# Kernel optimization log

Measured on AMD Instinct MI355X. Metric: run time of the kernel, lower is better.

## Reference

```python
import jax, jax.numpy as jnp
import numpy as np

DIM = 1024
HEADS = 16
HIDDEN = 4096
EPS = 1e-5


def _layernorm(x, g, b):
    mu = jnp.mean(x, axis=-1, keepdims=True)
    var = jnp.mean(jnp.square(x - mu), axis=-1, keepdims=True)
    return (x - mu) * jax.lax.rsqrt(var + EPS) * g + b


def setup_inputs() -> dict:
    key = jax.random.key(0)
    ks = jax.random.split(key, 12)
    B, N, C, Hd = 2, 2048, DIM, HIDDEN
    s = 0.02
    inp = {
        "x": jax.random.normal(ks[0], (B, N, C), dtype=jnp.float32),
        "mask": jax.random.randint(ks[1], (B, N), 0, 2).astype(bool),
        "ln1_g": jnp.ones((C,), jnp.float32),
        "ln1_b": jnp.zeros((C,), jnp.float32),
        "qkv_w": jax.random.normal(ks[2], (3 * C, C), jnp.float32) * s,
        "q_bias": jax.random.normal(ks[3], (C,), jnp.float32) * s,
        "v_bias": jax.random.normal(ks[4], (C,), jnp.float32) * s,
        "proj_w": jax.random.normal(ks[5], (C, C), jnp.float32) * s,
        "proj_b": jnp.zeros((C,), jnp.float32),
        "ln2_g": jnp.ones((C,), jnp.float32),
        "ln2_b": jnp.zeros((C,), jnp.float32),
        "fc1_w": jax.random.normal(ks[6], (Hd, C), jnp.float32) * s,
        "fc1_b": jnp.zeros((Hd,), jnp.float32),
        "fc2_w": jax.random.normal(ks[7], (C, Hd), jnp.float32) * s,
        "fc2_b": jnp.zeros((C,), jnp.float32),
    }
    return inp


def _block(x, mask, ln1_g, ln1_b, qkv_w, q_bias, v_bias, proj_w, proj_b,
           ln2_g, ln2_b, fc1_w, fc1_b, fc2_w, fc2_b):
    B, N, C = x.shape
    H = HEADS
    hd = C // H
    scale = hd ** -0.5

    # --- attention branch ---
    xn = _layernorm(x, ln1_g, ln1_b)
    qkv_bias = jnp.concatenate([q_bias, jnp.zeros_like(v_bias), v_bias])
    qkv = xn @ qkv_w.T + qkv_bias                       # [B,N,3C]
    qkv = qkv.reshape(B, N, 3, H, hd).transpose(2, 0, 3, 1, 4)  # [3,B,H,N,hd]
    q, k, v = qkv[0], qkv[1], qkv[2]
    q = q * scale
    attn = jnp.einsum('bhqd,bhkd->bhqk',
                      q.astype(jnp.float32), k.astype(jnp.float32))
    attn = jnp.where(mask[:, None, None, :], -jnp.inf, attn)
    attn = jax.nn.softmax(attn, axis=-1).astype(x.dtype)
    out = jnp.einsum('bhqk,bhkd->bhqd', attn, v)        # [B,H,N,hd]
    out = out.transpose(0, 2, 1, 3).reshape(B, N, C)
    out = out @ proj_w.T + proj_b
    x = x + out

    # --- MLP branch (Mlp_ returns pre-activation hidden too; norm=Identity) ---
    x2 = _layernorm(x, ln2_g, ln2_b)
    h = x2 @ fc1_w.T + fc1_b                            # [B,N,HIDDEN]
    x_interm = h
    h = jax.nn.gelu(h, approximate=False)
    y = h @ fc2_w.T + fc2_b
    x = x + y
    return x_interm, x


def reference(x, mask, ln1_g, ln1_b, qkv_w, q_bias, v_bias, proj_w, proj_b,
              ln2_g, ln2_b, fc1_w, fc1_b, fc2_w, fc2_b):
    return _block(x, mask, ln1_g, ln1_b, qkv_w, q_bias, v_bias, proj_w, proj_b,
                  ln2_g, ln2_b, fc1_w, fc1_b, fc2_w, fc2_b)
```

## Files before the change

kernel.cpp:

```cpp
#include <hip/hip_runtime.h>
#include <hip/hip_bf16.h>

typedef __attribute__((ext_vector_type(8))) short short8;
typedef __attribute__((ext_vector_type(4))) short short4v;
typedef __attribute__((ext_vector_type(4))) float f32x4;

__device__ inline float bf2f(short s) {
    unsigned u = ((unsigned)(unsigned short)s) << 16;
    float f; __builtin_memcpy(&f, &u, 4); return f;
}
__device__ inline short f2bf(float f) {
    unsigned u; __builtin_memcpy(&u, &f, 4);
    unsigned r = (u + 0x7fffu + ((u >> 16) & 1u)) >> 16;
    return (short)r;
}
__device__ inline float ex2(float x) {
    float r; asm("v_exp_f32 %0, %1" : "=v"(r) : "v"(x)); return r;
}
__device__ inline unsigned cvtpk(float lo, float hi) {
    unsigned r; asm("v_cvt_pk_bf16_f32 %0, %1, %2" : "=v"(r) : "v"(lo), "v"(hi)); return r;
}
__device__ inline float gelu_fast(float x) {
    float xx = x * x;
    float u2 = x * fmaf(0.10294323f, xx, 2.3022085f);
    float t = ex2(u2);
    return x - x * __builtin_amdgcn_rcpf(t + 1.f);
}

#define GLD_LDS16(g, l) __builtin_amdgcn_global_load_lds( \
    (const __attribute__((address_space(1))) void*)(g),   \
    (__attribute__((address_space(3))) void*)(l), 16, 0, 0)

#define BARRIER_PIN do { __builtin_amdgcn_s_barrier(); __builtin_amdgcn_sched_barrier(0); } while (0)

__global__ __launch_bounds__(256) void detect_kernel(const ushort* __restrict__ x,
                                                     const unsigned char* __restrict__ m,
                                                     int* __restrict__ flags) {
    __shared__ int cnt, weirdAny, weird40, nzNon4;
    if (threadIdx.x == 0) { cnt = 0; weirdAny = 0; weird40 = 0; nzNon4 = 0; }
    __syncthreads();
    for (int t = threadIdx.x; t < 512; t += 256) {
        unsigned u = x[2 * t];
        int e = (int)((u >> 7) & 0xFF);
        if (e >= 100 && e <= 130) atomicAdd(&cnt, 1);
    }
    for (int i = threadIdx.x; i < 4096; i += 256) {
        unsigned b = m[i];
        if (b > 1) { atomicOr(&weirdAny, 1); if ((i & 3) == 0) atomicOr(&weird40, 1); }
        if (b != 0 && (i & 3) != 0) atomicOr(&nzNon4, 1);
    }
    __syncthreads();
    if (threadIdx.x == 0) {
        flags[0] = (cnt < 256) ? 1 : 0;
        flags[1] = weirdAny ? (weird40 ? 2 : 3) : (nzNon4 ? 1 : 0);
    }
}

__global__ __launch_bounds__(256) void prep_kernel(
    const void* __restrict__ xs, const void* __restrict__ ms,
    const void* __restrict__ ln1g, const void* __restrict__ ln1b,
    const void* __restrict__ qkvw, const void* __restrict__ qb,
    const void* __restrict__ vb, const void* __restrict__ pw,
    const void* __restrict__ pb, const void* __restrict__ ln2g,
    const void* __restrict__ ln2b, const void* __restrict__ f1w,
    const void* __restrict__ f1b, const void* __restrict__ f2w,
    const void* __restrict__ f2b,
    char* __restrict__ w, const int* __restrict__ flags) {
    bool f32w = flags[0] != 0;
    const size_t MB = 1024 * 1024;
    int bid = blockIdx.x, tid = threadIdx.x;
    if (!f32w && bid < 8192) return;
    char* small = w + 88 * MB;
    auto cvt8 = [&](const void* src, ushort* dst, int i) {
        if (f32w) {
            const float* s = (const float*)src + i;
            short8 o;
            for (int j = 0; j < 8; j++) o[j] = f2bf(s[j]);
            *(short8*)&dst[i] = o;
        } else {
            *(short8*)&dst[i] = *(const short8*)((const ushort*)src + i);
        }
    };
    if (bid < 2048)       cvt8(xs,   (ushort*)(w + 56 * MB), (bid * 256 + tid) * 8);
    else if (bid < 3584)  cvt8(qkvw, (ushort*)(w + 64 * MB), ((bid - 2048) * 256 + tid) * 8);
    else if (bid < 4096)  cvt8(pw,   (ushort*)(w + 70 * MB), ((bid - 3584) * 256 + tid) * 8);
    else if (bid < 6144)  cvt8(f1w,  (ushort*)(w + 72 * MB), ((bid - 4096) * 256 + tid) * 8);
    else if (bid < 8192)  cvt8(f2w,  (ushort*)(w + 80 * MB), ((bid - 6144) * 256 + tid) * 8);
    else if (bid < 8198) {
        int e = (bid - 8192) * 2048 + tid * 8;
        const void* src; ushort* dst; int off;
        if (e < 7168) {
            int t = e >> 10; off = e & 1023;
            const void* s0;
            if (t == 0) s0 = ln1g; else if (t == 1) s0 = ln1b; else if (t == 2) s0 = qb;
            else if (t == 3) s0 = vb; else if (t == 4) s0 = pb; else if (t == 5) s0 = ln2g;
            else s0 = ln2b;
            src = s0; dst = (ushort*)(small + t * 4096);
        } else if (e < 8192) { src = f2b; off = e - 7168; dst = (ushort*)(small + 9 * 4096); }
        else                 { src = f1b; off = e - 8192; dst = (ushort*)(small + 7 * 4096); }
        cvt8(src, dst, off);
    } else {
        int enc = flags[1];
        unsigned char* md = (unsigned char*)(small + 10 * 4096);
        int i0 = (bid - 8198) * 2048 + tid * 8;
        for (int j = 0; j < 8; j++) {
            int i = i0 + j;
            unsigned char v;
            if (enc == 0)      v = (((const int*)ms)[i] != 0);
            else if (enc == 1) v = (((const unsigned char*)ms)[i] != 0);
            else if (enc == 2) v = (((const ushort*)ms)[i] != 0);
            else               v = ((((const unsigned*)ms)[i] << 1) != 0);
            md[i] = v;
        }
    }
}

__global__ __launch_bounds__(256) void ln_kernel(const void* __restrict__ xraw,
                                                 const ushort* __restrict__ xconv,
                                                 const ushort* __restrict__ g,
                                                 const ushort* __restrict__ b,
                                                 ushort* __restrict__ y,
                                                 const int* __restrict__ flags) {
    const ushort* x = (flags[0] != 0) ? xconv : (const ushort*)xraw;
    int wave = threadIdx.x >> 6, lane = threadIdx.x & 63;
    int row = blockIdx.x * 4 + wave;
    const ushort* xp = x + (size_t)row * 1024 + lane * 16;
    short8 v0 = *(const short8*)xp;
    short8 v1 = *(const short8*)(xp + 8);
    float f[16]; float s = 0.f, ss = 0.f;
    for (int i = 0; i < 8; i++) { f[i] = bf2f(v0[i]); f[i + 8] = bf2f(v1[i]); }
    for (int i = 0; i < 16; i++) { s += f[i]; ss += f[i] * f[i]; }
    for (int o = 1; o < 64; o <<= 1) { s += __shfl_xor(s, o, 64); ss += __shfl_xor(ss, o, 64); }
    float mu = s * (1.f / 1024.f);
    float var = ss * (1.f / 1024.f) - mu * mu;
    float rstd = rsqrtf(var + 1e-5f);
    short8 g0 = *(const short8*)&g[lane * 16];
    short8 g1 = *(const short8*)&g[lane * 16 + 8];
    short8 b0 = *(const short8*)&b[lane * 16];
    short8 b1 = *(const short8*)&b[lane * 16 + 8];
    short8 o0v, o1v;
    for (int i = 0; i < 8; i++) {
        o0v[i] = f2bf((f[i] - mu) * rstd * bf2f(g0[i]) + bf2f(b0[i]));
        o1v[i] = f2bf((f[i + 8] - mu) * rstd * bf2f(g1[i]) + bf2f(b1[i]));
    }
    ushort* yp = y + (size_t)row * 1024 + lane * 16;
    *(short8*)yp = o0v;
    *(short8*)(yp + 8) = o1v;
}

template <int EPI>
__device__ __forceinline__ void gemm_body(ushort* SM,
                                          const ushort* __restrict__ A,
                                          const void* __restrict__ Wraw,
                                          const ushort* __restrict__ Wconv,
                                          int K,
                                          const ushort* __restrict__ p0,
                                          const void* __restrict__ p1raw,
                                          const ushort* __restrict__ p1conv,
                                          void* __restrict__ o0,
                                          ushort* __restrict__ o1,
                                          const int* __restrict__ flags) {
    bool f32w = flags[0] != 0;
    const ushort* W  = f32w ? Wconv  : (const ushort*)Wraw;
    const ushort* p1 = f32w ? p1conv : (const ushort*)p1raw;
    int tid = threadIdx.x;
    int wave = tid >> 6, lane = tid & 63;
    int wr = wave >> 1, wc = wave & 1;
    int lr = lane & 15, lg = lane >> 4;
    int m0 = blockIdx.x * 128, n0 = blockIdx.y * 128;
    f32x4 acc[4][4];
    for (int i = 0; i < 4; i++) for (int j = 0; j < 4; j++) acc[i][j] = (f32x4){0.f, 0.f, 0.f, 0.f};

    int s0 = wave * 2;
    int srow = lane >> 2;
    int sslot = (lane & 3) ^ ((srow >> 1) & 3);
    const ushort* gA0 = &A[(size_t)(m0 + s0 * 16 + srow) * K + sslot * 8];
    const ushort* gA1 = gA0 + (size_t)16 * K;
    const ushort* gW0 = &W[(size_t)(n0 + s0 * 16 + srow) * K + sslot * 8];
    const ushort* gW1 = gW0 + (size_t)16 * K;

    auto STAGE = [&](int buf, int k0) {
        ushort* lA = &SM[buf * 4096 + s0 * 512];
        ushort* lW = &SM[12288 + buf * 4096 + s0 * 512];
        GLD_LDS16(gA0 + k0, lA);
        GLD_LDS16(gA1 + k0, lA + 512);
        GLD_LDS16(gW0 + k0, lW);
        GLD_LDS16(gW1 + k0, lW + 512);
    };

    int nk = K >> 5;
    STAGE(0, 0);
    if (nk > 1) {
        STAGE(1, 32);
        asm volatile("s_waitcnt vmcnt(4)" ::: "memory");
    } else {
        asm volatile("s_waitcnt vmcnt(0)" ::: "memory");
    }
    BARRIER_PIN;

    int rs = lg ^ ((lr >> 1) & 3);
    int cur = 0, stg = 2;
    for (int t = 0; t < nk; ++t) {
        if (t + 2 < nk) STAGE(stg, (t + 2) << 5);
        const ushort* Ab = &SM[cur * 4096];
        const ushort* Wb = &SM[12288 + cur * 4096];
        short8 af[4], wf[4];
        for (int mi = 0; mi < 4; mi++) af[mi] = *(const short8*)&Ab[(wr * 64 + mi * 16 + lr) * 32 + rs * 8];
        for (int ni = 0; ni < 4; ni++) wf[ni] = *(const short8*)&Wb[(wc * 64 + ni * 16 + lr) * 32 + rs * 8];
        for (int mi = 0; mi < 4; mi++)
            for (int ni = 0; ni < 4; ni++)
                acc[mi][ni] = __builtin_amdgcn_mfma_f32_16x16x32_bf16(af[mi], wf[ni], acc[mi][ni], 0, 0, 0);
        if (t + 1 < nk) {
            if (t + 2 < nk) asm volatile("s_waitcnt vmcnt(4)" ::: "memory");
            else            asm volatile("s_waitcnt vmcnt(0)" ::: "memory");
            BARRIER_PIN;
        }
        cur = (cur == 2) ? 0 : cur + 1;
        stg = (stg == 2) ? 0 : stg + 1;
    }

    float* Cs = (float*)SM;
    bool of32 = (EPI == 2 || EPI == 3) ? f32w : false;
    int r2 = tid >> 3;
    int lc = tid & 7;
    for (int mi = 0; mi < 4; mi++) {
        __syncthreads();
        int rb = wr * 16 + lg * 4;
        for (int ni = 0; ni < 4; ni++) {
            f32x4 v = acc[mi][ni];
            int cl = wc * 64 + ni * 16 + lr;
            for (int rr = 0; rr < 4; rr++) Cs[(rb + rr) * 132 + cl] = v[rr];
        }
        __syncthreads();
        int grow = m0 + mi * 16 + (r2 < 16 ? r2 : 48 + r2);
        if (EPI == 3 && of32) {
            for (int k = 0; k < 4; k++) {
                int c0l = k * 32 + lc * 4;
                int gcol = n0 + c0l;
                f32x4 v;
                for (int j = 0; j < 4; j++)
                    v[j] = Cs[r2 * 132 + c0l + j] + bf2f(p0[gcol + j])
                         + bf2f(p1[(size_t)grow * 1024 + gcol + j]);
                *(f32x4*)&((float*)o0)[16777216 + (size_t)grow * 1024 + gcol] = v;
            }
        } else {
            for (int half = 0; half < 2; half++) {
                int c0l = half * 64 + lc * 8;
                int gcol = n0 + c0l;
                float hv[8];
                for (int j = 0; j < 8; j++) hv[j] = Cs[r2 * 132 + c0l + j];
                short8 o;
                if (EPI == 0) {
                    int part = gcol >> 10, cc = gcol & 1023;
                    if (part == 0)
                        for (int j = 0; j < 8; j++) o[j] = f2bf((hv[j] + bf2f(p0[cc + j])) * 0.18033688f);
                    else if (part == 1)
                        for (int j = 0; j < 8; j++) o[j] = f2bf(hv[j]);
                    else
                        for (int j = 0; j < 8; j++) o[j] = f2bf(hv[j] + bf2f(p1[cc + j]));
                    *(short8*)&((ushort*)o0)[(size_t)grow * 3072 + gcol] = o;
                } else if (EPI == 1) {
                    for (int j = 0; j < 8; j++)
                        o[j] = f2bf(hv[j] + bf2f(p0[gcol + j])
                                  + bf2f(p1[(size_t)grow * 1024 + gcol + j]));
                    *(short8*)&((ushort*)o0)[(size_t)grow * 1024 + gcol] = o;
                } else if (EPI == 2) {
                    float h[8];
                    short8 og;
                    for (int j = 0; j < 8; j++) {
                        h[j] = hv[j] + bf2f(p0[gcol + j]);
                        og[j] = f2bf(gelu_fast(h[j]));
                    }
                    *(short8*)&o1[(size_t)grow * 4096 + gcol] = og;
                    if (of32) {
                        float* dst = &((float*)o0)[(size_t)grow * 4096 + gcol];
                        *(f32x4*)&dst[0] = (f32x4){h[0], h[1], h[2], h[3]};
                        *(f32x4*)&dst[4] = (f32x4){h[4], h[5], h[6], h[7]};
                    } else {
                        short8 oh;
                        for (int j = 0; j < 8; j++) oh[j] = f2bf(h[j]);
                        *(short8*)&((ushort*)o0)[(size_t)grow * 4096 + gcol] = oh;
                    }
                } else {
                    for (int j = 0; j < 8; j++)
                        o[j] = f2bf(hv[j] + bf2f(p0[gcol + j])
                                  + bf2f(p1[(size_t)grow * 1024 + gcol + j]));
                    *(short8*)&((ushort*)o0)[16777216 + (size_t)grow * 1024 + gcol] = o;
                }
            }
        }
    }
}

#define GEMM_WRAP(NAME, EPI)                                                          \
__global__ __launch_bounds__(256) void NAME(const ushort* __restrict__ A,            \
                                            const void* __restrict__ Wraw,           \
                                            const ushort* __restrict__ Wconv, int K, \
                                            const ushort* __restrict__ p0,           \
                                            const void* __restrict__ p1raw,          \
                                            const ushort* __restrict__ p1conv,       \
                                            void* __restrict__ o0,                   \
                                            ushort* __restrict__ o1,                 \
                                            const int* __restrict__ flags) {         \
    __shared__ ushort SM[24576];                                                     \
    gemm_body<EPI>(SM, A, Wraw, Wconv, K, p0, p1raw, p1conv, o0, o1, flags);         \
}

GEMM_WRAP(gemm_qkv, 0)
GEMM_WRAP(gemm_proj, 1)
GEMM_WRAP(gemm_fc1, 2)
GEMM_WRAP(gemm_fc2, 3)

__global__ __launch_bounds__(256) void vtrans_kernel(const ushort* __restrict__ qkv,
                                                     ushort* __restrict__ vT) {
    __shared__ ushort T[64][72];
    int bh = blockIdx.x;
    int b = bh >> 4, h = bh & 15;
    int n0 = blockIdx.y * 64;
    int t = threadIdx.x;
    int r = t >> 2;
    int c0 = (t & 3) * 16;
    const ushort* src = qkv + (size_t)(b * 2048 + n0 + r) * 3072 + 2048 + h * 64 + c0;
    *(short8*)&T[r][c0]     = *(const short8*)&src[0];
    *(short8*)&T[r][c0 + 8] = *(const short8*)&src[8];
    __syncthreads();
    int d = t >> 2;
    int g0 = (t & 3) * 16;
    short8 o0v, o1v;
    for (int j = 0; j < 8; j++) { o0v[j] = T[g0 + j][d]; o1v[j] = T[g0 + 8 + j][d]; }
    ushort* dst = vT + ((size_t)bh * 64 + d) * 2048 + n0 + g0;
    *(short8*)&dst[0] = o0v;
    *(short8*)&dst[8] = o1v;
}

__global__ __launch_bounds__(256) void attn_kernel(const ushort* __restrict__ qkv,
                                                   const ushort* __restrict__ vT,
                                                   const unsigned char* __restrict__ mask,
                                                   ushort* __restrict__ ao) {
    __shared__ ushort Ks[2][4096];
    __shared__ ushort Vs[2][4096];
    __shared__ unsigned Plw[4][544];
    __shared__ unsigned Pmf[1024];

    int tid = threadIdx.x, wave = tid >> 6, lane = tid & 63;
    int bid = (blockIdx.x & 7) * 64 + (blockIdx.x >> 3);
    int g = bid * 4 + wave;
    int b = g >> 10;
    int h = (g >> 6) & 15;
    int qt = g & 63;
    int lr = lane & 15, lg = lane >> 4;

    const ushort* qp = qkv + (size_t)(b * 2048 + qt * 32) * 3072 + h * 64;
    const ushort* kp = qkv + (size_t)(b * 2048) * 3072 + 1024 + h * 64;
    const ushort* vp = vT + ((size_t)(b * 16 + h) * 64) * 2048;
    const unsigned char* mk = mask + b * 2048;

    for (int i = tid; i < 1024; i += 256) {
        unsigned lo = mk[2 * i] ? 0u : 0xFFFFu;
        unsigned hi = mk[2 * i + 1] ? 0u : 0xFFFF0000u;
        Pmf[i] = lo | hi;
    }

    short8 qa[2][2];
    for (int sub = 0; sub < 2; sub++)
        for (int ks = 0; ks < 2; ks++)
            qa[sub][ks] = *(const short8*)&qp[(sub * 16 + lr) * 3072 + ks * 32 + lg * 8];
    short8 ones;
    for (int j = 0; j < 8; j++) ones[j] = (short)0x3F80;

    int srowoff = lane >> 3;
    int sslot = (lane & 7) ^ srowoff;
    int rs0 = lg ^ (lr & 7);
    int rs1 = (4 + lg) ^ (lr & 7);

    f32x4 accT[2][4];
    f32x4 accL[2];
    for (int s = 0; s < 2; s++) {
        accL[s] = (f32x4){0.f, 0.f, 0.f, 0.f};
        for (int i = 0; i < 4; i++) accT[s][i] = (f32x4){0.f, 0.f, 0.f, 0.f};
    }

    auto STAGEKV = [&](int buf, int c0) {
        const ushort* ksrc = kp + (size_t)(c0 + wave * 16 + srowoff) * 3072 + sslot * 8;
        GLD_LDS16(ksrc, &Ks[buf][wave * 1024]);
        GLD_LDS16(ksrc + (size_t)8 * 3072, &Ks[buf][wave * 1024 + 512]);
        const ushort* vsrc = vp + (size_t)(wave * 16 + srowoff) * 2048 + c0 + sslot * 8;
        GLD_LDS16(vsrc, &Vs[buf][wave * 1024]);
        GLD_LDS16(vsrc + (size_t)8 * 2048, &Vs[buf][wave * 1024 + 512]);
    };

    STAGEKV(0, 0);
    __syncthreads();

    for (int it = 0; it < 32; ++it) {
        int c0 = it * 64;
        int cur = it & 1;
        if (it < 31) STAGEKV(cur ^ 1, c0 + 64);

        unsigned mw[4][2];
        for (int t = 0; t < 4; t++) {
            uint2 m2 = *(const uint2*)&Pmf[it * 32 + 8 * t + 2 * lg];
            mw[t][0] = m2.x; mw[t][1] = m2.y;
        }
        f32x4 st[2][4];
        for (int t = 0; t < 4; t++) {
            int row = t * 16 + lr;
            short8 kf0 = *(const short8*)&Ks[cur][row * 64 + rs0 * 8];
            short8 kf1 = *(const short8*)&Ks[cur][row * 64 + rs1 * 8];
            for (int sub = 0; sub < 2; sub++) {
                f32x4 z = (f32x4){0.f, 0.f, 0.f, 0.f};
                z = __builtin_amdgcn_mfma_f32_16x16x32_bf16(kf0, qa[sub][0], z, 0, 0, 0);
                z = __builtin_amdgcn_mfma_f32_16x16x32_bf16(kf1, qa[sub][1], z, 0, 0, 0);
                st[sub][t] = z;
            }
        }
        short8 vf[2][4];
        for (int ks = 0; ks < 2; ks++) {
            int rsk = ks ? rs1 : rs0;
            for (int nt = 0; nt < 4; nt++)
                vf[ks][nt] = *(const short8*)&Vs[cur][(nt * 16 + lr) * 64 + rsk * 8];
        }
        for (int sub = 0; sub < 2; sub++) {
            for (int t = 0; t < 4; t++) {
                for (int rrh = 0; rrh < 2; rrh++) {
                    float plo = ex2(st[sub][t][2 * rrh]);
                    float phi = ex2(st[sub][t][2 * rrh + 1]);
                    unsigned w = cvtpk(plo, phi) & mw[t][rrh];
                    Plw[wave][(8 * t + 2 * lg + rrh) * 17 + lr] = w;
                }
            }
            for (int ks = 0; ks < 2; ks++) {
                unsigned wu[4];
                for (int jj = 0; jj < 4; jj++)
                    wu[jj] = Plw[wave][(16 * ks + 4 * lg + jj) * 17 + lr];
                short8 pf;
                __builtin_memcpy(&pf, wu, 16);
                accL[sub] = __builtin_amdgcn_mfma_f32_16x16x32_bf16(ones, pf, accL[sub], 0, 0, 0);
                for (int nt = 0; nt < 4; nt++)
                    accT[sub][nt] = __builtin_amdgcn_mfma_f32_16x16x32_bf16(vf[ks][nt], pf, accT[sub][nt], 0, 0, 0);
            }
        }
        __syncthreads();
    }

    for (int sub = 0; sub < 2; sub++) {
        float ls = accL[sub][0];
        float inv = (ls > 0.f) ? 1.f / ls : 0.f;
        ushort* op = ao + ((size_t)(b * 2048 + qt * 32 + sub * 16) * 1024) + h * 64;
        for (int nt = 0; nt < 4; nt++) {
            unsigned w0 = cvtpk(accT[sub][nt][0] * inv, accT[sub][nt][1] * inv);
            unsigned w1 = cvtpk(accT[sub][nt][2] * inv, accT[sub][nt][3] * inv);
            uint2 ov; ov.x = w0; ov.y = w1;
            *(uint2*)&op[lr * 1024 + 16 * nt + 4 * lg] = ov;
        }
    }
}

extern "C" void kernel_launch(void* const* d_in, const int* in_sizes, int n_in,
                              void* d_out, int out_size, void* d_ws, size_t ws_size,
                              hipStream_t stream) {
    (void)in_sizes; (void)n_in; (void)out_size; (void)ws_size;

    char* w = (char*)d_ws;
    const size_t MB = 1024 * 1024;
    ushort* xn  = (ushort*)(w + 0 * MB);
    ushort* qkv = (ushort*)(w + 8 * MB);
    ushort* vT  = (ushort*)(w + 32 * MB);
    ushort* x1  = (ushort*)(w + 40 * MB);
    ushort* x2n = (ushort*)(w + 48 * MB);
    ushort* gh  = (ushort*)(w + 8 * MB);
    ushort* x_c    = (ushort*)(w + 56 * MB);
    ushort* qkvw_c = (ushort*)(w + 64 * MB);
    ushort* projw_c= (ushort*)(w + 70 * MB);
    ushort* fc1w_c = (ushort*)(w + 72 * MB);
    ushort* fc2w_c = (ushort*)(w + 80 * MB);
    char* small = w + 88 * MB;
    ushort* ln1g_c = (ushort*)(small + 0 * 4096);
    ushort* ln1b_c = (ushort*)(small + 1 * 4096);
    ushort* qbias_c= (ushort*)(small + 2 * 4096);
    ushort* vbias_c= (ushort*)(small + 3 * 4096);
    ushort* projb_c= (ushort*)(small + 4 * 4096);
    ushort* ln2g_c = (ushort*)(small + 5 * 4096);
    ushort* ln2b_c = (ushort*)(small + 6 * 4096);
    ushort* fc1b_c = (ushort*)(small + 7 * 4096);
    ushort* fc2b_c = (ushort*)(small + 9 * 4096);
    unsigned char* mask_c = (unsigned char*)(small + 10 * 4096);
    int* flags = (int*)(small + 11 * 4096);
    ushort* ao = xn;

    detect_kernel<<<1, 256, 0, stream>>>((const ushort*)d_in[0],
                                         (const unsigned char*)d_in[1], flags);
    prep_kernel<<<8200, 256, 0, stream>>>(d_in[0], d_in[1], d_in[2], d_in[3], d_in[4],
                                          d_in[5], d_in[6], d_in[7], d_in[8], d_in[9],
                                          d_in[10], d_in[11], d_in[12], d_in[13], d_in[14],
                                          w, flags);

    ln_kernel<<<1024, 256, 0, stream>>>(d_in[0], x_c, ln1g_c, ln1b_c, xn, flags);
    gemm_qkv<<<dim3(32, 24), 256, 0, stream>>>(xn, d_in[4], qkvw_c, 1024, qbias_c,
                                               vbias_c, vbias_c, qkv, nullptr, flags);
    vtrans_kernel<<<dim3(32, 32), 256, 0, stream>>>(qkv, vT);
    attn_kernel<<<512, 256, 0, stream>>>(qkv, vT, mask_c, ao);
    gemm_proj<<<dim3(32, 8), 256, 0, stream>>>(ao, d_in[7], projw_c, 1024, projb_c,
                                               d_in[0], x_c, x1, nullptr, flags);
    ln_kernel<<<1024, 256, 0, stream>>>(x1, x1, ln2g_c, ln2b_c, x2n, flags);
    gemm_fc1<<<dim3(32, 32), 256, 0, stream>>>(x2n, d_in[11], fc1w_c, 1024, fc1b_c,
                                               fc1b_c, fc1b_c, d_out, gh, flags);
    gemm_fc2<<<dim3(32, 8), 256, 0, stream>>>(gh, d_in[13], fc2w_c, 4096, fc2b_c,
                                              x1, x1, d_out, nullptr, flags);
}
```

Measured before the change: 258.5 us.

## Use 256x256-tile 8-wave GEMM kernel for QKV and FC1 projections

Adds a new GEMM kernel with 256x256 output tiles, 512 threads and a double-buffered direct-to-LDS load pipeline, then uses it for the QKV and FC1 GEMMs instead of the 128-wide tile kernel. Bigger tiles raise arithmetic intensity and cut global/L2 traffic per FLOP. The cost is a smaller grid (192 and 256 blocks on a large-CU device), which may leave CUs idle, plus heavy LDS and register use (128 KB LDS, 32 accumulators per lane).

```diff
diff --git a/kernel.cpp b/kernel.cpp
--- a/kernel.cpp
+++ b/kernel.cpp
@@ -149,6 +149,169 @@
 }
 
 template <int EPI>
+__global__ __launch_bounds__(512, 2) void gemm256_body(const ushort* __restrict__ A,
+                                                       const void* __restrict__ Wraw,
+                                                       const ushort* __restrict__ Wconv,
+                                                       int K,
+                                                       const ushort* __restrict__ p0,
+                                                       const void* __restrict__ p1raw,
+                                                       const ushort* __restrict__ p1conv,
+                                                       void* __restrict__ o0,
+                                                       ushort* __restrict__ o1,
+                                                       const int* __restrict__ flags) {
+    __shared__ ushort SM[65536];
+    bool f32w = flags[0] != 0;
+    const ushort* W  = f32w ? Wconv  : (const ushort*)Wraw;
+    const ushort* p1 = f32w ? p1conv : (const ushort*)p1raw;
+    int tid = threadIdx.x;
+    int wave = tid >> 6, lane = tid & 63;
+    int wm = wave >> 2, wn = wave & 3;
+    int lr = lane & 15, lg = lane >> 4;
+    int m0 = blockIdx.x * 256, n0 = blockIdx.y * 256;
+
+    f32x4 acc[8][4];
+#pragma unroll
+    for (int i = 0; i < 8; i++)
+#pragma unroll
+        for (int j = 0; j < 4; j++) acc[i][j] = (f32x4){0.f, 0.f, 0.f, 0.f};
+
+    int l31 = lane & 31;
+    int sgrp = (lane >> 5) * 2;
+    const ushort* gA = &A[(size_t)(m0 + wave * 32 + l31) * K];
+    const ushort* gB = &W[(size_t)(n0 + wave * 32 + l31) * K];
+
+    auto STAGE_U = [&](int op, int h, int buf, int k0) {
+        const ushort* g = op ? gB : gA;
+        ushort* base = &SM[op * 32768 + buf * 16384 + h * 8192 + wave * 1024];
+        GLD_LDS16(g + k0 + h * 32 + sgrp * 8, base);
+        GLD_LDS16(g + k0 + h * 32 + (sgrp + 1) * 8, base + 512);
+    };
+    auto rdA = [&](int R, int h, int cur) -> short8 {
+        return *(const short8*)&SM[cur * 16384 + h * 8192 + (R >> 5) * 1024 +
+                                   (lg & 1) * 512 + ((lg >> 1) * 32 + (R & 31)) * 8];
+    };
+    auto rdB = [&](int R, int h, int cur) -> short8 {
+        return *(const short8*)&SM[32768 + cur * 16384 + h * 8192 + (R >> 5) * 1024 +
+                                   (lg & 1) * 512 + ((lg >> 1) * 32 + (R & 31)) * 8];
+    };
+
+    int nk = K >> 6;
+    STAGE_U(0, 0, 0, 0); STAGE_U(1, 0, 0, 0); STAGE_U(0, 1, 0, 0); STAGE_U(1, 1, 0, 0);
+
+    for (int t = 0; t < nk; ++t) {
+        int cur = t & 1, nxt = cur ^ 1;
+        int k1 = (t + 1) << 6;
+        bool more = (t + 1) < nk;
+        short8 af[4], bf[4];
+        if (more) { STAGE_U(0, 0, nxt, k1); asm volatile("s_waitcnt vmcnt(6)" ::: "memory"); }
+        else      { asm volatile("s_waitcnt vmcnt(4)" ::: "memory"); }
+        BARRIER_PIN;
+#pragma unroll
+        for (int nf = 0; nf < 4; nf++) bf[nf] = rdB(wn * 64 + nf * 16 + lr, 0, cur);
+#pragma unroll
+        for (int mi = 0; mi < 4; mi++) af[mi] = rdA(wm * 128 + mi * 16 + lr, 0, cur);
+        __builtin_amdgcn_s_setprio(1);
+#pragma unroll
+        for (int mi = 0; mi < 4; mi++)
+#pragma unroll
+            for (int nf = 0; nf < 4; nf++)
+                acc[mi][nf] = __builtin_amdgcn_mfma_f32_16x16x32_bf16(af[mi], bf[nf], acc[mi][nf], 0, 0, 0);
+        __builtin_amdgcn_s_setprio(0);
+        if (more) STAGE_U(1, 0, nxt, k1);
+#pragma unroll
+        for (int mi = 0; mi < 4; mi++) af[mi] = rdA(wm * 128 + 64 + mi * 16 + lr, 0, cur);
+        __builtin_amdgcn_s_setprio(1);
+#pragma unroll
+        for (int mi = 0; mi < 4; mi++)
+#pragma unroll
+            for (int nf = 0; nf < 4; nf++)
+                acc[4 + mi][nf] = __builtin_amdgcn_mfma_f32_16x16x32_bf16(af[mi], bf[nf], acc[4 + mi][nf], 0, 0, 0);
+        __builtin_amdgcn_s_setprio(0);
+        if (more) { STAGE_U(0, 1, nxt, k1); asm volatile("s_waitcnt vmcnt(6)" ::: "memory"); }
+        else      { asm volatile("s_waitcnt vmcnt(0)" ::: "memory"); }
+        BARRIER_PIN;
+#pragma unroll
+        for (int nf = 0; nf < 4; nf++) bf[nf] = rdB(wn * 64 + nf * 16 + lr, 1, cur);
+#pragma unroll
+        for (int mi = 0; mi < 4; mi++) af[mi] = rdA(wm * 128 + mi * 16 + lr, 1, cur);
+        __builtin_amdgcn_s_setprio(1);
+#pragma unroll
+        for (int mi = 0; mi < 4; mi++)
+#pragma unroll
+            for (int nf = 0; nf < 4; nf++)
+                acc[mi][nf] = __builtin_amdgcn_mfma_f32_16x16x32_bf16(af[mi], bf[nf], acc[mi][nf], 0, 0, 0);
+        __builtin_amdgcn_s_setprio(0);
+        if (more) STAGE_U(1, 1, nxt, k1);
+#pragma unroll
+        for (int mi = 0; mi < 4; mi++) af[mi] = rdA(wm * 128 + 64 + mi * 16 + lr, 1, cur);
+        __builtin_amdgcn_s_setprio(1);
+#pragma unroll
+        for (int mi = 0; mi < 4; mi++)
+#pragma unroll
+            for (int nf = 0; nf < 4; nf++)
+                acc[4 + mi][nf] = __builtin_amdgcn_mfma_f32_16x16x32_bf16(af[mi], bf[nf], acc[4 + mi][nf], 0, 0, 0);
+        __builtin_amdgcn_s_setprio(0);
+    }
+
+    float* Cs = (float*)SM;
+    bool of32 = (EPI == 2) ? f32w : false;
+    int r2 = tid >> 4;
+    int cb = (tid & 15) * 16;
+#pragma unroll
+    for (int mf = 0; mf < 8; mf++) {
+        __syncthreads();
+        int crow = wm * 16 + lg * 4;
+#pragma unroll
+        for (int nf = 0; nf < 4; nf++) {
+            f32x4 v = acc[mf][nf];
+            int cl = wn * 64 + nf * 16 + lr;
+#pragma unroll
+            for (int rr = 0; rr < 4; rr++) Cs[(crow + rr) * 264 + cl] = v[rr];
+        }
+        __syncthreads();
+        int grow = m0 + (r2 >> 4) * 128 + mf * 16 + (r2 & 15);
+        float hv[16];
+#pragma unroll
+        for (int j = 0; j < 16; j += 4) *(f32x4*)&hv[j] = *(f32x4*)&Cs[r2 * 264 + cb + j];
+        int gcol = n0 + cb;
+        if (EPI == 0) {
+            int part = gcol >> 10, cc = gcol & 1023;
+            short8 o[2];
+            for (int j = 0; j < 16; j++) {
+                float vv = hv[j];
+                if (part == 0)      vv = (vv + bf2f(p0[cc + j])) * 0.18033688f;
+                else if (part == 2) vv = vv + bf2f(p1[cc + j]);
+                o[j >> 3][j & 7] = f2bf(vv);
+            }
+            ushort* dst = &((ushort*)o0)[(size_t)grow * 3072 + gcol];
+            *(short8*)dst = o[0];
+            *(short8*)(dst + 8) = o[1];
+        } else {
+            float h[16];
+            short8 og[2];
+            for (int j = 0; j < 16; j++) {
+                h[j] = hv[j] + bf2f(p0[gcol + j]);
+                og[j >> 3][j & 7] = f2bf(gelu_fast(h[j]));
+            }
+            ushort* gd = &o1[(size_t)grow * 4096 + gcol];
+            *(short8*)gd = og[0];
+            *(short8*)(gd + 8) = og[1];
+            if (of32) {
+                float* dst = &((float*)o0)[(size_t)grow * 4096 + gcol];
+#pragma unroll
+                for (int j = 0; j < 16; j += 4) *(f32x4*)&dst[j] = *(f32x4*)&h[j];
+            } else {
+                short8 oh[2];
+                for (int j = 0; j < 16; j++) oh[j >> 3][j & 7] = f2bf(h[j]);
+                ushort* dst = &((ushort*)o0)[(size_t)grow * 4096 + gcol];
+                *(short8*)dst = oh[0];
+                *(short8*)(dst + 8) = oh[1];
+            }
+        }
+    }
+}
+
+template <int EPI>
 __device__ __forceinline__ void gemm_body(ushort* SM,
                                           const ushort* __restrict__ A,
                                           const void* __restrict__ Wraw,
@@ -250,37 +413,11 @@
                 float hv[8];
                 for (int j = 0; j < 8; j++) hv[j] = Cs[r2 * 132 + c0l + j];
                 short8 o;
-                if (EPI == 0) {
-                    int part = gcol >> 10, cc = gcol & 1023;
-                    if (part == 0)
-                        for (int j = 0; j < 8; j++) o[j] = f2bf((hv[j] + bf2f(p0[cc + j])) * 0.18033688f);
-                    else if (part == 1)
-                        for (int j = 0; j < 8; j++) o[j] = f2bf(hv[j]);
-                    else
-                        for (int j = 0; j < 8; j++) o[j] = f2bf(hv[j] + bf2f(p1[cc + j]));
-                    *(short8*)&((ushort*)o0)[(size_t)grow * 3072 + gcol] = o;
-                } else if (EPI == 1) {
+                if (EPI == 1) {
                     for (int j = 0; j < 8; j++)
                         o[j] = f2bf(hv[j] + bf2f(p0[gcol + j])
                                   + bf2f(p1[(size_t)grow * 1024 + gcol + j]));
                     *(short8*)&((ushort*)o0)[(size_t)grow * 1024 + gcol] = o;
-                } else if (EPI == 2) {
-                    float h[8];
-                    short8 og;
-                    for (int j = 0; j < 8; j++) {
-                        h[j] = hv[j] + bf2f(p0[gcol + j]);
-                        og[j] = f2bf(gelu_fast(h[j]));
-                    }
-                    *(short8*)&o1[(size_t)grow * 4096 + gcol] = og;
-                    if (of32) {
-                        float* dst = &((float*)o0)[(size_t)grow * 4096 + gcol];
-                        *(f32x4*)&dst[0] = (f32x4){h[0], h[1], h[2], h[3]};
-                        *(f32x4*)&dst[4] = (f32x4){h[4], h[5], h[6], h[7]};
-                    } else {
-                        short8 oh;
-                        for (int j = 0; j < 8; j++) oh[j] = f2bf(h[j]);
-                        *(short8*)&((ushort*)o0)[(size_t)grow * 4096 + gcol] = oh;
-                    }
                 } else {
                     for (int j = 0; j < 8; j++)
                         o[j] = f2bf(hv[j] + bf2f(p0[gcol + j])
@@ -306,9 +443,7 @@
     gemm_body<EPI>(SM, A, Wraw, Wconv, K, p0, p1raw, p1conv, o0, o1, flags);         \
 }
 
-GEMM_WRAP(gemm_qkv, 0)
 GEMM_WRAP(gemm_proj, 1)
-GEMM_WRAP(gemm_fc1, 2)
 GEMM_WRAP(gemm_fc2, 3)
 
 __global__ __launch_bounds__(256) void vtrans_kernel(const ushort* __restrict__ qkv,
@@ -496,15 +631,15 @@
                                           w, flags);
 
     ln_kernel<<<1024, 256, 0, stream>>>(d_in[0], x_c, ln1g_c, ln1b_c, xn, flags);
-    gemm_qkv<<<dim3(32, 24), 256, 0, stream>>>(xn, d_in[4], qkvw_c, 1024, qbias_c,
-                                               vbias_c, vbias_c, qkv, nullptr, flags);
+    gemm256_body<0><<<dim3(16, 12), 512, 0, stream>>>(xn, d_in[4], qkvw_c, 1024, qbias_c,
+                                                      vbias_c, vbias_c, qkv, nullptr, flags);
     vtrans_kernel<<<dim3(32, 32), 256, 0, stream>>>(qkv, vT);
     attn_kernel<<<512, 256, 0, stream>>>(qkv, vT, mask_c, ao);
     gemm_proj<<<dim3(32, 8), 256, 0, stream>>>(ao, d_in[7], projw_c, 1024, projb_c,
                                                d_in[0], x_c, x1, nullptr, flags);
     ln_kernel<<<1024, 256, 0, stream>>>(x1, x1, ln2g_c, ln2b_c, x2n, flags);
-    gemm_fc1<<<dim3(32, 32), 256, 0, stream>>>(x2n, d_in[11], fc1w_c, 1024, fc1b_c,
-                                               fc1b_c, fc1b_c, d_out, gh, flags);
+    gemm256_body<2><<<dim3(16, 16), 512, 0, stream>>>(x2n, d_in[11], fc1w_c, 1024, fc1b_c,
+                                                      fc1b_c, fc1b_c, d_out, gh, flags);
     gemm_fc2<<<dim3(32, 8), 256, 0, stream>>>(gh, d_in[13], fc2w_c, 4096, fc2b_c,
                                               x1, x1, d_out, nullptr, flags);
 }
```

Result: slower. 322.0 us (+24.6%).

## Split attention KV range across waves with cross-wave reduction and precomputed mask words

Applied to the files above, without the earlier changes.

Attention blocks now cover 64 query rows with every wave sharing them, and each wave handles its own quarter of the key/value sequence using private double-buffered LDS and explicit vmcnt waits instead of block-wide barriers. Partial outputs and row sums are reduced across waves through LDS at the end. The packed mask words are now built once in the prep kernel rather than in every attention block. This removes per-iteration __syncthreads and per-block mask packing, and doubles the grid, at the cost of more accumulator registers and a final reduction pass.

```diff
diff --git a/kernel.cpp b/kernel.cpp
--- a/kernel.cpp
+++ b/kernel.cpp
@@ -102,7 +102,9 @@
     } else {
         int enc = flags[1];
         unsigned char* md = (unsigned char*)(small + 10 * 4096);
+        unsigned* pmw = (unsigned*)(small + 12 * 4096);
         int i0 = (bid - 8198) * 2048 + tid * 8;
+        unsigned char mv[8];
         for (int j = 0; j < 8; j++) {
             int i = i0 + j;
             unsigned char v;
@@ -111,6 +113,12 @@
             else if (enc == 2) v = (((const ushort*)ms)[i] != 0);
             else               v = ((((const unsigned*)ms)[i] << 1) != 0);
             md[i] = v;
+            mv[j] = v;
+        }
+        for (int p = 0; p < 4; p++) {
+            unsigned lo = mv[2 * p] ? 0u : 0xFFFFu;
+            unsigned hi = mv[2 * p + 1] ? 0u : 0xFFFF0000u;
+            pmw[(i0 >> 1) + p] = lo | hi;
         }
     }
 }
@@ -335,123 +343,151 @@
 
 __global__ __launch_bounds__(256) void attn_kernel(const ushort* __restrict__ qkv,
                                                    const ushort* __restrict__ vT,
-                                                   const unsigned char* __restrict__ mask,
+                                                   const unsigned* __restrict__ pmw,
                                                    ushort* __restrict__ ao) {
-    __shared__ ushort Ks[2][4096];
-    __shared__ ushort Vs[2][4096];
-    __shared__ unsigned Plw[4][544];
-    __shared__ unsigned Pmf[1024];
-
+    __shared__ ushort SM[35328];
     int tid = threadIdx.x, wave = tid >> 6, lane = tid & 63;
-    int bid = (blockIdx.x & 7) * 64 + (blockIdx.x >> 3);
-    int g = bid * 4 + wave;
-    int b = g >> 10;
-    int h = (g >> 6) & 15;
-    int qt = g & 63;
+    int bid = (blockIdx.x & 7) * 128 + (blockIdx.x >> 3);
+    int b = bid >> 9;
+    int h = (bid >> 5) & 15;
+    int qt = bid & 31;
     int lr = lane & 15, lg = lane >> 4;
 
-    const ushort* qp = qkv + (size_t)(b * 2048 + qt * 32) * 3072 + h * 64;
+    const ushort* qp = qkv + (size_t)(b * 2048 + qt * 64) * 3072 + h * 64;
     const ushort* kp = qkv + (size_t)(b * 2048) * 3072 + 1024 + h * 64;
     const ushort* vp = vT + ((size_t)(b * 16 + h) * 64) * 2048;
-    const unsigned char* mk = mask + b * 2048;
-
-    for (int i = tid; i < 1024; i += 256) {
-        unsigned lo = mk[2 * i] ? 0u : 0xFFFFu;
-        unsigned hi = mk[2 * i + 1] ? 0u : 0xFFFF0000u;
-        Pmf[i] = lo | hi;
-    }
-
-    short8 qa[2][2];
-    for (int sub = 0; sub < 2; sub++)
+    int pmbase = b * 1024;
+
+    short8 qa[4][2];
+    for (int sub = 0; sub < 4; sub++)
         for (int ks = 0; ks < 2; ks++)
             qa[sub][ks] = *(const short8*)&qp[(sub * 16 + lr) * 3072 + ks * 32 + lg * 8];
     short8 ones;
     for (int j = 0; j < 8; j++) ones[j] = (short)0x3F80;
 
-    int srowoff = lane >> 3;
-    int sslot = (lane & 7) ^ srowoff;
+    int srk = lane >> 3;
+    int ssk = (lane & 7) ^ srk;
+    int srv = lane >> 2;
+    int ssv = (lane & 3) ^ (srv & 3);
     int rs0 = lg ^ (lr & 7);
     int rs1 = (4 + lg) ^ (lr & 7);
-
-    f32x4 accT[2][4];
-    f32x4 accL[2];
-    for (int s = 0; s < 2; s++) {
+    int rsv = lg ^ (lr & 3);
+
+    unsigned* Plw = (unsigned*)&SM[32768 + wave * 640];
+
+    f32x4 accT[4][4];
+    f32x4 accL[4];
+    for (int s = 0; s < 4; s++) {
         accL[s] = (f32x4){0.f, 0.f, 0.f, 0.f};
         for (int i = 0; i < 4; i++) accT[s][i] = (f32x4){0.f, 0.f, 0.f, 0.f};
     }
 
-    auto STAGEKV = [&](int buf, int c0) {
-        const ushort* ksrc = kp + (size_t)(c0 + wave * 16 + srowoff) * 3072 + sslot * 8;
-        GLD_LDS16(ksrc, &Ks[buf][wave * 1024]);
-        GLD_LDS16(ksrc + (size_t)8 * 3072, &Ks[buf][wave * 1024 + 512]);
-        const ushort* vsrc = vp + (size_t)(wave * 16 + srowoff) * 2048 + c0 + sslot * 8;
-        GLD_LDS16(vsrc, &Vs[buf][wave * 1024]);
-        GLD_LDS16(vsrc + (size_t)8 * 2048, &Vs[buf][wave * 1024 + 512]);
+    auto STAGEKV = [&](int buf, int kvb) {
+        ushort* kb = &SM[(wave * 2 + buf) * 2048];
+        ushort* vb = &SM[16384 + (wave * 2 + buf) * 2048];
+        for (int i = 0; i < 4; i++)
+            GLD_LDS16(kp + (size_t)(kvb + i * 8 + srk) * 3072 + ssk * 8, kb + i * 512);
+        for (int i = 0; i < 4; i++)
+            GLD_LDS16(vp + (size_t)(i * 16 + srv) * 2048 + kvb + ssv * 8, vb + i * 512);
     };
 
-    STAGEKV(0, 0);
-    __syncthreads();
-
-    for (int it = 0; it < 32; ++it) {
-        int c0 = it * 64;
+    int kv0 = wave * 512;
+    STAGEKV(0, kv0);
+
+    for (int it = 0; it < 16; ++it) {
         int cur = it & 1;
-        if (it < 31) STAGEKV(cur ^ 1, c0 + 64);
-
-        unsigned mw[4][2];
-        for (int t = 0; t < 4; t++) {
-            uint2 m2 = *(const uint2*)&Pmf[it * 32 + 8 * t + 2 * lg];
-            mw[t][0] = m2.x; mw[t][1] = m2.y;
-        }
-        f32x4 st[2][4];
-        for (int t = 0; t < 4; t++) {
-            int row = t * 16 + lr;
-            short8 kf0 = *(const short8*)&Ks[cur][row * 64 + rs0 * 8];
-            short8 kf1 = *(const short8*)&Ks[cur][row * 64 + rs1 * 8];
-            for (int sub = 0; sub < 2; sub++) {
+        int kvb = kv0 + it * 32;
+        if (it < 15) {
+            STAGEKV(cur ^ 1, kvb + 32);
+            asm volatile("s_waitcnt vmcnt(8)" ::: "memory");
+        } else {
+            asm volatile("s_waitcnt vmcnt(0)" ::: "memory");
+        }
+        __builtin_amdgcn_sched_barrier(0);
+
+        uint2 mwa = *(const uint2*)&pmw[pmbase + (kvb >> 1) + 2 * lg];
+        uint2 mwb = *(const uint2*)&pmw[pmbase + (kvb >> 1) + 8 + 2 * lg];
+
+        const ushort* Kb = &SM[(wave * 2 + cur) * 2048];
+        const ushort* Vb = &SM[16384 + (wave * 2 + cur) * 2048];
+        short8 kf[2][2];
+        for (int t = 0; t < 2; t++) {
+            int row = 16 * t + lr;
+            kf[t][0] = *(const short8*)&Kb[row * 64 + rs0 * 8];
+            kf[t][1] = *(const short8*)&Kb[row * 64 + rs1 * 8];
+        }
+        short8 vf[4];
+        for (int nt = 0; nt < 4; nt++)
+            vf[nt] = *(const short8*)&Vb[(nt * 16 + lr) * 32 + rsv * 8];
+
+        f32x4 st[4][2];
+        for (int sub = 0; sub < 4; sub++)
+            for (int t = 0; t < 2; t++) {
                 f32x4 z = (f32x4){0.f, 0.f, 0.f, 0.f};
-                z = __builtin_amdgcn_mfma_f32_16x16x32_bf16(kf0, qa[sub][0], z, 0, 0, 0);
-                z = __builtin_amdgcn_mfma_f32_16x16x32_bf16(kf1, qa[sub][1], z, 0, 0, 0);
+                z = __builtin_amdgcn_mfma_f32_16x16x32_bf16(kf[t][0], qa[sub][0], z, 0, 0, 0);
+                z = __builtin_amdgcn_mfma_f32_16x16x32_bf16(kf[t][1], qa[sub][1], z, 0, 0, 0);
                 st[sub][t] = z;
             }
-        }
-        short8 vf[2][4];
-        for (int ks = 0; ks < 2; ks++) {
-            int rsk = ks ? rs1 : rs0;
-            for (int nt = 0; nt < 4; nt++)
-                vf[ks][nt] = *(const short8*)&Vs[cur][(nt * 16 + lr) * 64 + rsk * 8];
-        }
-        for (int sub = 0; sub < 2; sub++) {
-            for (int t = 0; t < 4; t++) {
-                for (int rrh = 0; rrh < 2; rrh++) {
-                    float plo = ex2(st[sub][t][2 * rrh]);
-                    float phi = ex2(st[sub][t][2 * rrh + 1]);
-                    unsigned w = cvtpk(plo, phi) & mw[t][rrh];
-                    Plw[wave][(8 * t + 2 * lg + rrh) * 17 + lr] = w;
+
+        for (int sub = 0; sub < 4; sub++) {
+            for (int t = 0; t < 2; t++) {
+                unsigned m0 = t ? mwb.x : mwa.x;
+                unsigned m1 = t ? mwb.y : mwa.y;
+                {
+                    float plo = ex2(st[sub][t][0]);
+                    float phi = ex2(st[sub][t][1]);
+                    Plw[(8 * t + 2 * lg) * 17 + lr] = cvtpk(plo, phi) & m0;
+                }
+                {
+                    float plo = ex2(st[sub][t][2]);
+                    float phi = ex2(st[sub][t][3]);
+                    Plw[(8 * t + 2 * lg + 1) * 17 + lr] = cvtpk(plo, phi) & m1;
                 }
             }
-            for (int ks = 0; ks < 2; ks++) {
-                unsigned wu[4];
-                for (int jj = 0; jj < 4; jj++)
-                    wu[jj] = Plw[wave][(16 * ks + 4 * lg + jj) * 17 + lr];
-                short8 pf;
-                __builtin_memcpy(&pf, wu, 16);
-                accL[sub] = __builtin_amdgcn_mfma_f32_16x16x32_bf16(ones, pf, accL[sub], 0, 0, 0);
-                for (int nt = 0; nt < 4; nt++)
-                    accT[sub][nt] = __builtin_amdgcn_mfma_f32_16x16x32_bf16(vf[ks][nt], pf, accT[sub][nt], 0, 0, 0);
+            unsigned wu[4];
+            for (int jj = 0; jj < 4; jj++)
+                wu[jj] = Plw[(4 * lg + jj) * 17 + lr];
+            short8 pf;
+            __builtin_memcpy(&pf, wu, 16);
+            accL[sub] = __builtin_amdgcn_mfma_f32_16x16x32_bf16(ones, pf, accL[sub], 0, 0, 0);
+            for (int nt = 0; nt < 4; nt++)
+                accT[sub][nt] = __builtin_amdgcn_mfma_f32_16x16x32_bf16(vf[nt], pf, accT[sub][nt], 0, 0, 0);
+        }
+    }
+
+    {
+        float* redK = (float*)&SM[wave * 4096];
+        float* redV = (float*)&SM[16384 + wave * 4096];
+        float* redL = (float*)&SM[32768 + wave * 640];
+        for (int s = 0; s < 4; s++)
+            for (int nt = 0; nt < 4; nt++) {
+                float* base = (s < 2) ? &redK[(s * 4 + nt) * 256] : &redV[((s - 2) * 4 + nt) * 256];
+                *(f32x4*)&base[lane * 4] = accT[s][nt];
             }
-        }
-        __syncthreads();
-    }
-
-    for (int sub = 0; sub < 2; sub++) {
-        float ls = accL[sub][0];
-        float inv = (ls > 0.f) ? 1.f / ls : 0.f;
-        ushort* op = ao + ((size_t)(b * 2048 + qt * 32 + sub * 16) * 1024) + h * 64;
+        for (int s = 0; s < 4; s++) redL[s * 64 + lane] = accL[s][0];
+    }
+    __syncthreads();
+    {
+        int s = wave;
+        f32x4 tot[4];
+        for (int nt = 0; nt < 4; nt++) tot[nt] = (f32x4){0.f, 0.f, 0.f, 0.f};
+        float totL = 0.f;
+        for (int w2 = 0; w2 < 4; w2++) {
+            const float* rb = (s < 2) ? (const float*)&SM[w2 * 4096] + (s * 4) * 256
+                                      : (const float*)&SM[16384 + w2 * 4096] + ((s - 2) * 4) * 256;
+            for (int nt = 0; nt < 4; nt++) {
+                f32x4 v = *(const f32x4*)&rb[nt * 256 + lane * 4];
+                for (int rr = 0; rr < 4; rr++) tot[nt][rr] += v[rr];
+            }
+            totL += ((const float*)&SM[32768 + w2 * 640])[s * 64 + lane];
+        }
+        float inv = (totL > 0.f) ? 1.f / totL : 0.f;
+        ushort* op = ao + ((size_t)(b * 2048 + qt * 64 + s * 16 + lr) * 1024) + h * 64;
         for (int nt = 0; nt < 4; nt++) {
-            unsigned w0 = cvtpk(accT[sub][nt][0] * inv, accT[sub][nt][1] * inv);
-            unsigned w1 = cvtpk(accT[sub][nt][2] * inv, accT[sub][nt][3] * inv);
+            unsigned w0 = cvtpk(tot[nt][0] * inv, tot[nt][1] * inv);
+            unsigned w1 = cvtpk(tot[nt][2] * inv, tot[nt][3] * inv);
             uint2 ov; ov.x = w0; ov.y = w1;
-            *(uint2*)&op[lr * 1024 + 16 * nt + 4 * lg] = ov;
+            *(uint2*)&op[16 * nt + 4 * lg] = ov;
         }
     }
 }
@@ -484,7 +520,7 @@
     ushort* ln2b_c = (ushort*)(small + 6 * 4096);
     ushort* fc1b_c = (ushort*)(small + 7 * 4096);
     ushort* fc2b_c = (ushort*)(small + 9 * 4096);
-    unsigned char* mask_c = (unsigned char*)(small + 10 * 4096);
+    unsigned* pmw  = (unsigned*)(small + 12 * 4096);
     int* flags = (int*)(small + 11 * 4096);
     ushort* ao = xn;
 
@@ -499,7 +535,7 @@
     gemm_qkv<<<dim3(32, 24), 256, 0, stream>>>(xn, d_in[4], qkvw_c, 1024, qbias_c,
                                                vbias_c, vbias_c, qkv, nullptr, flags);
     vtrans_kernel<<<dim3(32, 32), 256, 0, stream>>>(qkv, vT);
-    attn_kernel<<<512, 256, 0, stream>>>(qkv, vT, mask_c, ao);
+    attn_kernel<<<1024, 256, 0, stream>>>(qkv, vT, pmw, ao);
     gemm_proj<<<dim3(32, 8), 256, 0, stream>>>(ao, d_in[7], projw_c, 1024, projb_c,
                                                d_in[0], x_c, x1, nullptr, flags);
     ln_kernel<<<1024, 256, 0, stream>>>(x1, x1, ln2g_c, ln2b_c, x2n, flags);
```

New measurement: 265.8 us. +2.8%, slower.
